# Optimization experiments

Hardware: AMD Instinct MI355X
Metric: run time of the kernel (lower is better)

Reference implementation:

```python
import jax, jax.numpy as jnp
import numpy as np

B, T, C = 4, 2048, 2048
H, N = 32, 64          # n_head, head_size; H*N == C (n_dim_att == n_dim)
DMIX, DDEC = 32, 64    # hardcoded LoRA dims in module


def setup_inputs() -> dict:
    key = jax.random.key(0)
    ks = jax.random.split(key, 24)
    u = lambda k, s, lo, hi: jax.random.uniform(k, s, jnp.float32, lo, hi)
    g = lambda k, s: jax.random.normal(k, s, jnp.float32) * 0.02
    return {
        'x': jax.random.normal(ks[0], (B, T, C), jnp.float32),
        'shift_state_in': jax.random.normal(ks[1], (B, C), jnp.float32),
        'wkv_state_in': jnp.zeros((B, H, N, N), jnp.float32),
        'time_maa_x': u(ks[2], (C,), 0.0, 1.0),
        'time_maa_r': u(ks[3], (C,), 0.0, 1.0),
        'time_maa_k': u(ks[4], (C,), 0.0, 1.0),
        'time_maa_v': u(ks[5], (C,), 0.0, 1.0),
        'time_maa_w': u(ks[6], (C,), 0.0, 1.0),
        'time_maa_v2': u(ks[7], (C,), 0.0, 1.0),
        'time_maa_w1': u(ks[8], (C, DMIX * 5), -0.01, 0.01),
        'time_maa_w2': u(ks[9], (5, DMIX, C), -0.01, 0.01),
        'time_decay': u(ks[10], (C,), -6.0, -1.0),
        'time_decay_w1': u(ks[11], (C, DDEC), -0.01, 0.01),
        'time_decay_w2': u(ks[12], (DDEC, C), -0.01, 0.01),
        'time_value2_w1': u(ks[13], (C, DDEC), -0.01, 0.01),
        'time_value2_w2': u(ks[14], (DDEC, C), -0.01, 0.01),
        'W_r': g(ks[15], (C, C)),
        'W_k': g(ks[16], (C, C)),
        'W_v': g(ks[17], (C, C)),
        'W_o': g(ks[18], (C, C)),
        'ln_w': jnp.ones((C,), jnp.float32),
        'ln_b': jnp.zeros((C,), jnp.float32),
    }


def _to_heads(a):
    # [B,T,C] -> [T,B,H,N] for time-major scan
    return a.reshape(B, T, H, N).transpose(1, 0, 2, 3)


def reference(x, shift_state_in, wkv_state_in,
              time_maa_x, time_maa_r, time_maa_k, time_maa_v, time_maa_w, time_maa_v2,
              time_maa_w1, time_maa_w2,
              time_decay, time_decay_w1, time_decay_w2,
              time_value2_w1, time_value2_w2,
              W_r, W_k, W_v, W_o, ln_w, ln_b):
    # token shift
    dxprev = jnp.concatenate([shift_state_in[:, None, :], x[:, :-1]], axis=1) - x
    xxx = x + dxprev * time_maa_x
    hmix = jnp.tanh(xxx @ time_maa_w1).reshape(B, T, 5, DMIX)
    mix = jnp.einsum('btfd,fdc->fbtc', hmix, time_maa_w2)  # [5,B,T,C]
    mr, mk, mv, mw, mv2 = mix
    xr = x + dxprev * (time_maa_r + mr)
    xk = x + dxprev * (time_maa_k + mk)
    xv = x + dxprev * (time_maa_v + mv)
    xw = x + dxprev * (time_maa_w + mw)
    xv2 = x + dxprev * (time_maa_v2 + mv2)

    r = xr @ W_r
    k = xk @ W_k
    v = xv @ W_v
    v2 = xv2 @ W_v + jnp.tanh(xv2 @ time_value2_w1) @ time_value2_w2
    w = time_decay + jnp.tanh(xw @ time_decay_w1) @ time_decay_w2
    decay = jnp.exp(-jnp.exp(w))         # per-channel, data-dependent
    k = k * (1.0 - decay)

    rh, kh, vh, dh = _to_heads(r), _to_heads(k), _to_heads(v), _to_heads(decay)

    def step(state, inputs):
        # state: [B,H,N,N] (k-dim x v-dim); u (time_faaaa) is zero in this variant
        r_t, k_t, v_t, d_t = inputs  # each [B,H,N]
        y = jnp.einsum('bhi,bhij->bhj', r_t, state)
        state = state * d_t[..., None] + k_t[..., None] * v_t[..., None, :]
        return state, y

    wkv_state_out, ys = jax.lax.scan(step, wkv_state_in, (rh, kh, vh, dh))
    y = ys.transpose(1, 0, 2, 3).reshape(B, T, C)
    y = y + v2
    # LayerNorm over n_dim_att
    mu = jnp.mean(y, axis=-1, keepdims=True)
    var = jnp.var(y, axis=-1, keepdims=True)
    y = (y - mu) / jnp.sqrt(var + 1e-5) * ln_w + ln_b
    y = y @ W_o
    return y, x[:, -1], wkv_state_out
```

## Files before the change

### kernel.cpp

```cpp
#include <hip/hip_runtime.h>
#include <hip/hip_bf16.h>
#include <cstdio>


typedef __attribute__((ext_vector_type(8))) short bf16x8;
typedef __attribute__((ext_vector_type(4))) float floatx4;

#define T_DIM 2048
#define C_DIM 2048
#define B_DIM 4
#define M_ROWS (B_DIM * T_DIM)

typedef const unsigned int __attribute__((address_space(1)))* gas1_t;
typedef unsigned int __attribute__((address_space(3)))* las3_t;
__device__ __forceinline__ void gl_lds16(const void* g, void* l) {
    __builtin_amdgcn_global_load_lds((gas1_t)g, (las3_t)l, 16, 0, 0);
}

__global__ __launch_bounds__(256) void k_transpose(
    const float* __restrict__ in, void* __restrict__ out,
    int R, int Cin, int to_bf16)
{
    __shared__ float tile[32][33];
    const int tx = threadIdx.x & 31, ty = threadIdx.x >> 5;
    const int cbase = blockIdx.x * 32, rbase = blockIdx.y * 32;
#pragma unroll
    for (int i = 0; i < 4; i++) {
        int r = rbase + ty + i * 8;
        int c = cbase + tx;
        tile[ty + i * 8][tx] = (c < Cin) ? in[(size_t)r * Cin + c] : 0.0f;
    }
    __syncthreads();
    if (to_bf16) {
        __hip_bfloat16* ob = (__hip_bfloat16*)out;
#pragma unroll
        for (int i = 0; i < 4; i++) {
            int c = cbase + ty + i * 8;
            ob[(size_t)c * R + rbase + tx] = __float2bfloat16(tile[tx][ty + i * 8]);
        }
    } else {
        float* of = (float*)out;
#pragma unroll
        for (int i = 0; i < 4; i++) {
            int c = cbase + ty + i * 8;
            of[(size_t)c * R + rbase + tx] = tile[tx][ty + i * 8];
        }
    }
}

__global__ __launch_bounds__(256) void k_xx(
    const float* __restrict__ x, const float* __restrict__ shift,
    const float* __restrict__ tmx,
    __hip_bfloat16* __restrict__ XX, float* __restrict__ xlast)
{
    const int row = blockIdx.x;
    const int b = row >> 11, t = row & 2047;
    const int c0 = threadIdx.x * 8;
    const float* xrow = x + (size_t)row * C_DIM;
    const float* prow = (t == 0) ? (shift + (size_t)b * C_DIM) : (xrow - C_DIM);
    float4 xa = ((const float4*)(xrow + c0))[0];
    float4 xb = ((const float4*)(xrow + c0))[1];
    float4 pa = ((const float4*)(prow + c0))[0];
    float4 pb = ((const float4*)(prow + c0))[1];
    float xv8[8] = {xa.x, xa.y, xa.z, xa.w, xb.x, xb.y, xb.z, xb.w};
    float pv8[8] = {pa.x, pa.y, pa.z, pa.w, pb.x, pb.y, pb.z, pb.w};
    union { bf16x8 v8; __hip_bfloat16 e[8]; } u;
#pragma unroll
    for (int j = 0; j < 8; j++)
        u.e[j] = __float2bfloat16(fmaf(pv8[j] - xv8[j], tmx[c0 + j], xv8[j]));
    *(bf16x8*)(XX + (size_t)row * C_DIM + c0) = u.v8;
    if (t == T_DIM - 1) {
        ((float4*)(xlast + (size_t)b * C_DIM + c0))[0] = xa;
        ((float4*)(xlast + (size_t)b * C_DIM + c0))[1] = xb;
    }
}

__global__ __launch_bounds__(256) void k_gemm_h(
    const __hip_bfloat16* __restrict__ A,
    const __hip_bfloat16* __restrict__ Bt,
    __hip_bfloat16* __restrict__ Hout)
{
    __shared__ __hip_bfloat16 As[64 * 32];
    __shared__ __hip_bfloat16 Bs[256 * 32];
    const int tid = threadIdx.x;
    const int m0 = blockIdx.x * 64;
    const int wave = tid >> 6, lane = tid & 63;
    const int fcol = lane & 15, quad = lane >> 4;
    floatx4 acc[16];
#pragma unroll
    for (int i = 0; i < 16; i++) acc[i] = (floatx4){0.f, 0.f, 0.f, 0.f};

    const int rA = tid >> 2, kcA = (tid & 3) * 8;
    const __hip_bfloat16* gA = A + (size_t)(m0 + rA) * 2048 + kcA;
    __hip_bfloat16* lA = As + tid * 8;
    const __hip_bfloat16* gB[4];
    __hip_bfloat16* lB[4];
#pragma unroll
    for (int s = 0; s < 4; s++) {
        int q = tid + 256 * s;
        gB[s] = Bt + (size_t)(q >> 2) * 2048 + (q & 3) * 8;
        lB[s] = Bs + q * 8;
    }
    for (int kk = 0; kk < 2048; kk += 32) {
        gl_lds16(gA + kk, lA);
#pragma unroll
        for (int s = 0; s < 4; s++) gl_lds16(gB[s] + kk, lB[s]);
        __syncthreads();
        bf16x8 aF = *(const bf16x8*)(As + (wave * 16 + fcol) * 32 + quad * 8);
#pragma unroll
        for (int ni = 0; ni < 16; ni++) {
            bf16x8 bF = *(const bf16x8*)(Bs + (ni * 16 + fcol) * 32 + quad * 8);
            acc[ni] = __builtin_amdgcn_mfma_f32_16x16x32_bf16(aF, bF, acc[ni], 0, 0, 0);
        }
        __syncthreads();
    }
#pragma unroll
    for (int ni = 0; ni < 16; ni++) {
        int col = ni * 16 + fcol;
#pragma unroll
        for (int g = 0; g < 4; g++) {
            int row = m0 + wave * 16 + quad * 4 + g;
            Hout[(size_t)row * 256 + col] = __float2bfloat16(tanhf(acc[ni][g]));
        }
    }
}

__global__ __launch_bounds__(256) void k_gemm_n64(
    const __hip_bfloat16* __restrict__ A,
    const __hip_bfloat16* __restrict__ Bt,
    __hip_bfloat16* __restrict__ G)
{
    __shared__ __hip_bfloat16 As[64 * 32];
    __shared__ __hip_bfloat16 Bs[64 * 32];
    const int tid = threadIdx.x;
    const int m0 = blockIdx.x * 64;
    const int wave = tid >> 6, lane = tid & 63;
    const int fcol = lane & 15, quad = lane >> 4;
    floatx4 acc[4];
#pragma unroll
    for (int i = 0; i < 4; i++) acc[i] = (floatx4){0.f, 0.f, 0.f, 0.f};

    const int r = tid >> 2, kc = (tid & 3) * 8;
    const __hip_bfloat16* gA = A + (size_t)(m0 + r) * 2048 + kc;
    const __hip_bfloat16* gB = Bt + (size_t)r * 2048 + kc;
    __hip_bfloat16* lA = As + tid * 8;
    __hip_bfloat16* lB = Bs + tid * 8;
    for (int kk = 0; kk < 2048; kk += 32) {
        gl_lds16(gA + kk, lA);
        gl_lds16(gB + kk, lB);
        __syncthreads();
        bf16x8 aF = *(const bf16x8*)(As + (wave * 16 + fcol) * 32 + quad * 8);
#pragma unroll
        for (int ni = 0; ni < 4; ni++) {
            bf16x8 bF = *(const bf16x8*)(Bs + (ni * 16 + fcol) * 32 + quad * 8);
            acc[ni] = __builtin_amdgcn_mfma_f32_16x16x32_bf16(aF, bF, acc[ni], 0, 0, 0);
        }
        __syncthreads();
    }
#pragma unroll
    for (int ni = 0; ni < 4; ni++) {
        int col = ni * 16 + fcol;
#pragma unroll
        for (int g = 0; g < 4; g++) {
            int row = m0 + wave * 16 + quad * 4 + g;
            G[(size_t)row * 64 + col] = __float2bfloat16(tanhf(acc[ni][g]));
        }
    }
}

__global__ __launch_bounds__(256) void k_mixfused(
    const float* __restrict__ x, const float* __restrict__ shift,
    const __hip_bfloat16* __restrict__ Hb,
    const __hip_bfloat16* __restrict__ w2T,
    const float* __restrict__ tmr, const float* __restrict__ tmk,
    const float* __restrict__ tmv, const float* __restrict__ tmw,
    const float* __restrict__ tmv2,
    __hip_bfloat16* __restrict__ xr, __hip_bfloat16* __restrict__ xk,
    __hip_bfloat16* __restrict__ xv, __hip_bfloat16* __restrict__ xw,
    __hip_bfloat16* __restrict__ xv2)
{
    __shared__ float          xp[33 * 256];
    __shared__ __hip_bfloat16 Hs[32 * 256];
    __shared__ __hip_bfloat16 mixS[32 * 256];

    const int tid = threadIdx.x;
    const int bid = blockIdx.x;
    const int n0 = (bid & 7) * 256;
    const int m0 = (bid >> 3) * 32;
    const int wave = tid >> 6, lane = tid & 63;
    const int fcol = lane & 15, quad = lane >> 4;
    const int wm = (wave >> 1) * 16, wn = (wave & 1) * 128;

#pragma unroll
    for (int i = 0; i < 8; i++) {
        int row = i * 4 + wave;
        gl_lds16(x + (size_t)(m0 + row) * C_DIM + n0 + lane * 4,
                 xp + (row + 1) * 256 + lane * 4);
    }
    if (wave == 0) {
        const float* src = (m0 & 2047)
            ? (x + (size_t)(m0 - 1) * C_DIM + n0)
            : (shift + (size_t)(m0 >> 11) * C_DIM + n0);
        gl_lds16(src + lane * 4, xp + lane * 4);
    }
#pragma unroll
    for (int i = 0; i < 4; i++) {
        int q = tid + 256 * i;
        gl_lds16(Hb + (size_t)(m0 + (q >> 5)) * 256 + (q & 31) * 8,
                 Hs + (q >> 5) * 256 + (q & 31) * 8);
    }
    asm volatile("s_waitcnt vmcnt(0) lgkmcnt(0)" ::: "memory");
    __builtin_amdgcn_s_barrier();
    __builtin_amdgcn_sched_barrier(0);

    const float* maas[5] = {tmr, tmk, tmv, tmw, tmv2};
    __hip_bfloat16* outs[5] = {xr, xk, xv, xw, xv2};
    const int cc = tid & 31, c0 = cc * 8, rb = tid >> 5;

#pragma unroll
    for (int f = 0; f < 5; f++) {
        {
            bf16x8 aF = *(const bf16x8*)(Hs + (wm + fcol) * 256 + f * 32 + quad * 8);
            floatx4 acc[8];
#pragma unroll
            for (int nf = 0; nf < 8; nf++) {
                bf16x8 bF = *(const bf16x8*)(
                    w2T + (size_t)(n0 + wn + nf * 16 + fcol) * 160 + f * 32 + quad * 8);
                acc[nf] = __builtin_amdgcn_mfma_f32_16x16x32_bf16(
                    aF, bF, (floatx4){0.f, 0.f, 0.f, 0.f}, 0, 0, 0);
            }
#pragma unroll
            for (int nf = 0; nf < 8; nf++)
#pragma unroll
                for (int g = 0; g < 4; g++)
                    mixS[(wm + quad * 4 + g) * 256 + wn + nf * 16 + fcol] =
                        __float2bfloat16(acc[nf][g]);
        }
        asm volatile("s_waitcnt lgkmcnt(0)" ::: "memory");
        __builtin_amdgcn_s_barrier();
        __builtin_amdgcn_sched_barrier(0);

        {
            float4 ma = ((const float4*)(maas[f] + n0 + c0))[0];
            float4 mb = ((const float4*)(maas[f] + n0 + c0))[1];
            float m8[8] = {ma.x, ma.y, ma.z, ma.w, mb.x, mb.y, mb.z, mb.w};
#pragma unroll
            for (int i = 0; i < 4; i++) {
                int row = rb + 8 * i;
                float4 xa = ((const float4*)(xp + (row + 1) * 256 + c0))[0];
                float4 xb = ((const float4*)(xp + (row + 1) * 256 + c0))[1];
                float4 pa = ((const float4*)(xp + row * 256 + c0))[0];
                float4 pb = ((const float4*)(xp + row * 256 + c0))[1];
                float xv8[8] = {xa.x, xa.y, xa.z, xa.w, xb.x, xb.y, xb.z, xb.w};
                float pv8[8] = {pa.x, pa.y, pa.z, pa.w, pb.x, pb.y, pb.z, pb.w};
                union { bf16x8 v8; __hip_bfloat16 e[8]; } mu;
                mu.v8 = *(const bf16x8*)(mixS + row * 256 + c0);
                union { bf16x8 v8; __hip_bfloat16 e[8]; } u;
#pragma unroll
                for (int j = 0; j < 8; j++) {
                    float dx = pv8[j] - xv8[j];
                    float mixv = __bfloat162float(mu.e[j]);
                    u.e[j] = __float2bfloat16(fmaf(dx, m8[j] + mixv, xv8[j]));
                }
                *(bf16x8*)(outs[f] + (size_t)(m0 + row) * C_DIM + n0 + c0) = u.v8;
            }
        }
        if (f < 4) {
            asm volatile("s_waitcnt lgkmcnt(0)" ::: "memory");
            __builtin_amdgcn_s_barrier();
            __builtin_amdgcn_sched_barrier(0);
        }
    }
}

__global__ __launch_bounds__(512, 2) void k_gemm256(
    const __hip_bfloat16* __restrict__ A,
    const __hip_bfloat16* __restrict__ Bt,
    int mode,
    float* __restrict__ outF, __hip_bfloat16* __restrict__ outB)
{
    constexpr int K = 2048;
    constexpr int NT = K / 32;
    __shared__ __hip_bfloat16 LA[4][256 * 32];
    __shared__ __hip_bfloat16 LB[4][256 * 32];
    const int tid = threadIdx.x;
    const int bid = blockIdx.x;
    const int n0 = (bid & 7) * 256;
    const int m0 = (bid >> 3) * 256;
    const int wave = tid >> 6, lane = tid & 63;
    const int wm = (wave >> 2) * 128, wn = (wave & 3) * 64;
    const int fcol = lane & 15, quad = lane >> 4;

    floatx4 acc[8][4];
#pragma unroll
    for (int mi = 0; mi < 8; mi++)
#pragma unroll
        for (int ni = 0; ni < 4; ni++)
            acc[mi][ni] = (floatx4){0.f, 0.f, 0.f, 0.f};

    const int ch0 = wave * 2, ch1 = wave * 2 + 1;
    const int rr = lane >> 2, kc = (lane & 3) * 8;
    const __hip_bfloat16* pA0 = A  + (size_t)(m0 + ch0 * 16 + rr) * K + kc;
    const __hip_bfloat16* pA1 = A  + (size_t)(m0 + ch1 * 16 + rr) * K + kc;
    const __hip_bfloat16* pB0 = Bt + (size_t)(n0 + ch0 * 16 + rr) * K + kc;
    const __hip_bfloat16* pB1 = Bt + (size_t)(n0 + ch1 * 16 + rr) * K + kc;
    const int lo0 = ch0 * 512 + lane * 8;
    const int lo1 = ch1 * 512 + lane * 8;

    int ns = 0;
    for (; ns < 3; ++ns) {
        gl_lds16(pA0 + ns * 32, &LA[ns][lo0]);
        gl_lds16(pA1 + ns * 32, &LA[ns][lo1]);
        gl_lds16(pB0 + ns * 32, &LB[ns][lo0]);
        gl_lds16(pB1 + ns * 32, &LB[ns][lo1]);
    }
    for (int t = 0; t < NT; ++t) {
        if (t < NT - 2)       asm volatile("s_waitcnt vmcnt(8)" ::: "memory");
        else if (t == NT - 2) asm volatile("s_waitcnt vmcnt(4)" ::: "memory");
        else                  asm volatile("s_waitcnt vmcnt(0)" ::: "memory");
        asm volatile("s_barrier" ::: "memory");
        if (ns < NT) {
            const int sl = ns & 3;
            gl_lds16(pA0 + ns * 32, &LA[sl][lo0]);
            gl_lds16(pA1 + ns * 32, &LA[sl][lo1]);
            gl_lds16(pB0 + ns * 32, &LB[sl][lo0]);
            gl_lds16(pB1 + ns * 32, &LB[sl][lo1]);
            ++ns;
        }
        const int st = t & 3;
        const __hip_bfloat16* ab = &LA[st][(wm + fcol) * 32 + quad * 8];
        const __hip_bfloat16* bb = &LB[st][(wn + fcol) * 32 + quad * 8];
        bf16x8 bF[4];
#pragma unroll
        for (int ni = 0; ni < 4; ni++)
            bF[ni] = *(const bf16x8*)(bb + ni * 512);
#pragma unroll
        for (int mi = 0; mi < 8; mi++) {
            bf16x8 aF = *(const bf16x8*)(ab + mi * 512);
#pragma unroll
            for (int ni = 0; ni < 4; ni++)
                acc[mi][ni] = __builtin_amdgcn_mfma_f32_16x16x32_bf16(
                    aF, bF[ni], acc[mi][ni], 0, 0, 0);
        }
    }
#pragma unroll
    for (int mi = 0; mi < 8; mi++) {
#pragma unroll
        for (int ni = 0; ni < 4; ni++) {
            int rbase = m0 + wm + mi * 16 + quad * 4;
            int ccol = n0 + wn + ni * 16 + fcol;
#pragma unroll
            for (int g = 0; g < 4; g++) {
                size_t idx = (size_t)(rbase + g) * 2048 + ccol;
                float val = acc[mi][ni][g];
                if (mode == 0) outF[idx] = val;
                else           outB[idx] = __float2bfloat16(val);
            }
        }
    }
}

__global__ __launch_bounds__(256) void k_gemm64(
    const __hip_bfloat16* __restrict__ A0, const __hip_bfloat16* __restrict__ B0,
    const __hip_bfloat16* __restrict__ A1, const __hip_bfloat16* __restrict__ B1,
    float* __restrict__ decayOut, const float* __restrict__ tdec,
    __hip_bfloat16* __restrict__ v2Out)
{
    constexpr int K = 64;
    __shared__ __hip_bfloat16 As[128 * 32];
    __shared__ __hip_bfloat16 Bs[128 * 32];
    const int tid = threadIdx.x;
    const int op = blockIdx.x >> 10;
    const int id = blockIdx.x & 1023;
    const int xcd = id & 7, jj = id >> 3;
    const int m0 = (((xcd << 3) | (jj & 7))) * 128;
    const int n0 = (jj >> 3) * 128;
    const __hip_bfloat16* A = op ? A1 : A0;
    const __hip_bfloat16* Bt = op ? B1 : B0;
    const int wave = tid >> 6, lane = tid & 63;
    const int wm = (wave >> 1) * 64, wn = (wave & 1) * 64;
    const int fcol = lane & 15, quad = lane >> 4;

    floatx4 acc[4][4];
#pragma unroll
    for (int mi = 0; mi < 4; mi++)
#pragma unroll
        for (int ni = 0; ni < 4; ni++)
            acc[mi][ni] = (floatx4){0.f, 0.f, 0.f, 0.f};

    const int q0 = tid, q1 = tid + 256;
    const int r0 = q0 >> 2, kc0 = (q0 & 3) * 8;
    const int r1 = q1 >> 2, kc1 = (q1 & 3) * 8;
    const __hip_bfloat16* gA0 = A + (size_t)(m0 + r0) * K + kc0;
    const __hip_bfloat16* gA1 = A + (size_t)(m0 + r1) * K + kc1;
    const __hip_bfloat16* gB0 = Bt + (size_t)(n0 + r0) * K + kc0;
    const __hip_bfloat16* gB1 = Bt + (size_t)(n0 + r1) * K + kc1;
    __hip_bfloat16* lA0 = As + q0 * 8; __hip_bfloat16* lA1 = As + q1 * 8;
    __hip_bfloat16* lB0 = Bs + q0 * 8; __hip_bfloat16* lB1 = Bs + q1 * 8;

    for (int kk = 0; kk < K; kk += 32) {
        gl_lds16(gA0 + kk, lA0);
        gl_lds16(gA1 + kk, lA1);
        gl_lds16(gB0 + kk, lB0);
        gl_lds16(gB1 + kk, lB1);
        __syncthreads();
        bf16x8 aF[4], bF[4];
#pragma unroll
        for (int mi = 0; mi < 4; mi++)
            aF[mi] = *(const bf16x8*)(As + (wm + mi * 16 + fcol) * 32 + quad * 8);
#pragma unroll
        for (int ni = 0; ni < 4; ni++)
            bF[ni] = *(const bf16x8*)(Bs + (wn + ni * 16 + fcol) * 32 + quad * 8);
#pragma unroll
        for (int mi = 0; mi < 4; mi++)
#pragma unroll
            for (int ni = 0; ni < 4; ni++)
                acc[mi][ni] = __builtin_amdgcn_mfma_f32_16x16x32_bf16(
                    aF[mi], bF[ni], acc[mi][ni], 0, 0, 0);
        __syncthreads();
    }
#pragma unroll
    for (int mi = 0; mi < 4; mi++) {
#pragma unroll
        for (int ni = 0; ni < 4; ni++) {
            int rbase = m0 + wm + mi * 16 + quad * 4;
            int ccol = n0 + wn + ni * 16 + fcol;
#pragma unroll
            for (int g = 0; g < 4; g++) {
                size_t idx = (size_t)(rbase + g) * 2048 + ccol;
                float val = acc[mi][ni][g];
                if (op == 0) {
                    decayOut[idx] = expf(-expf(val + tdec[ccol]));
                } else {
                    v2Out[idx] = __float2bfloat16(__bfloat162float(v2Out[idx]) + val);
                }
            }
        }
    }
}

__global__ __launch_bounds__(256) void k_scan_chunked(
    const __hip_bfloat16* __restrict__ r, const __hip_bfloat16* __restrict__ k,
    const __hip_bfloat16* __restrict__ v, const float* __restrict__ dec,
    const float* __restrict__ state_in,
    __hip_bfloat16* __restrict__ y, float* __restrict__ state_out)
{
    __shared__ __hip_bfloat16 Rs[2][64 * 64];
    __shared__ __hip_bfloat16 Ks[2][64 * 64];
    __shared__ __hip_bfloat16 Vs[2][64 * 64];
    __shared__ float          Dsb[2][64 * 64];
    __shared__ __hip_bfloat16 Ys[2][64 * 64];
    __shared__ __hip_bfloat16 Am[64 * 72];
    __shared__ __hip_bfloat16 Bm[64 * 72];
    __shared__ __hip_bfloat16 VT[64 * 72];
    __shared__ __hip_bfloat16 CT[64 * 72];
    __shared__ __hip_bfloat16 ST[64 * 72];
    __shared__ __hip_bfloat16 Pm[64 * 72];
    __shared__ float part[4][64];
    __shared__ float efin[64];

    const int tid = threadIdx.x;
    const int bh = blockIdx.x, b = bh >> 5, h = bh & 31;
    const int wave = tid >> 6, lane = tid & 63;
    const int fcol = lane & 15, quad = lane >> 4;
    const int ci = tid & 63, seg = tid >> 6;

    floatx4 sfr[4];
    {
        const float* sp = state_in + (size_t)bh * 4096;
#pragma unroll
        for (int n = 0; n < 4; n++)
#pragma unroll
            for (int g = 0; g < 4; g++)
                sfr[n][g] = sp[(size_t)(16 * wave + quad * 4 + g) * 64 + 16 * n + fcol];
    }

    const size_t cbase0 = (size_t)b * T_DIM * C_DIM + (size_t)h * 64;

    auto stage = [&](int cc, int buf) {
        const size_t cb = cbase0 + (size_t)cc * 64 * C_DIM;
        const int q0 = tid, q1 = tid + 256;
        const size_t o0 = (size_t)(q0 >> 3) * C_DIM + (q0 & 7) * 8;
        const size_t o1 = (size_t)(q1 >> 3) * C_DIM + (q1 & 7) * 8;
        gl_lds16(r + cb + o0, &Rs[buf][q0 * 8]);
        gl_lds16(r + cb + o1, &Rs[buf][q1 * 8]);
        gl_lds16(k + cb + o0, &Ks[buf][q0 * 8]);
        gl_lds16(k + cb + o1, &Ks[buf][q1 * 8]);
        gl_lds16(v + cb + o0, &Vs[buf][q0 * 8]);
        gl_lds16(v + cb + o1, &Vs[buf][q1 * 8]);
        gl_lds16(y + cb + o0, &Ys[buf][q0 * 8]);
        gl_lds16(y + cb + o1, &Ys[buf][q1 * 8]);
#pragma unroll
        for (int s = 0; s < 4; s++) {
            int q = tid + 256 * s;
            gl_lds16(dec + cb + (size_t)(q >> 4) * C_DIM + (q & 15) * 4,
                     &Dsb[buf][q * 4]);
        }
    };

    stage(0, 0);

    for (int c = 0; c < 32; c++) {
        const int cur = c & 1, nxt = cur ^ 1;
        const size_t cb = cbase0 + (size_t)c * 64 * C_DIM;

        if (c == 0) asm volatile("s_waitcnt vmcnt(0)" ::: "memory");
        else        asm volatile("s_waitcnt vmcnt(16)" ::: "memory");
        asm volatile("s_waitcnt lgkmcnt(0)" ::: "memory");
        __builtin_amdgcn_s_barrier();
        __builtin_amdgcn_sched_barrier(0);

        if (c + 1 < 32) stage(c + 1, nxt);

        {
#pragma unroll
            for (int n = 0; n < 4; n++)
#pragma unroll
                for (int g = 0; g < 4; g++)
                    ST[(size_t)(16 * n + fcol) * 72 + 16 * wave + quad * 4 + g] =
                        __float2bfloat16(sfr[n][g]);
            float p = 1.0f;
#pragma unroll
            for (int u = 0; u < 16; u++) p *= Dsb[cur][(seg * 16 + u) * 64 + ci];
            part[seg][ci] = p;
        }
        asm volatile("s_waitcnt lgkmcnt(0)" ::: "memory");
        __builtin_amdgcn_s_barrier();
        __builtin_amdgcn_sched_barrier(0);

        {
            float p0 = part[0][ci], p1 = part[1][ci], p2 = part[2][ci], p3 = part[3][ci];
            float pre = 1.0f;
            if (seg > 0) pre *= p0;
            if (seg > 1) pre *= p1;
            if (seg > 2) pre *= p2;
            float tot = p0 * p1 * p2 * p3;
            if (seg == 0) efin[ci] = tot;
            float e = pre;
#pragma unroll
            for (int u = 0; u < 16; u++) {
                int t = seg * 16 + u;
                float d = Dsb[cur][t * 64 + ci];
                float rv = __bfloat162float(Rs[cur][t * 64 + ci]);
                float kv = __bfloat162float(Ks[cur][t * 64 + ci]) * (1.0f - d);
                Am[t * 72 + ci] = __float2bfloat16(rv * e);
                e *= d;
                float bb = kv * __builtin_amdgcn_rcpf(e);
                Bm[t * 72 + ci] = __float2bfloat16(bb);
                CT[ci * 72 + t] = __float2bfloat16(bb * tot);
            }
#pragma unroll
            for (int u = 0; u < 16; u++) {
                int t = seg * 16 + ((u + (ci & 15)) & 15);
                VT[ci * 72 + t] = Vs[cur][t * 64 + ci];
            }
        }
        asm volatile("s_waitcnt lgkmcnt(0)" ::: "memory");
        __builtin_amdgcn_s_barrier();
        __builtin_amdgcn_sched_barrier(0);

        {
            bf16x8 af[2];
#pragma unroll
            for (int kk = 0; kk < 2; kk++)
                af[kk] = *(const bf16x8*)(Am + (16 * wave + fcol) * 72 + kk * 32 + quad * 8);
            floatx4 pfr[4], yfr[4];
#pragma unroll
            for (int n = 0; n < 4; n++) {
                pfr[n] = (floatx4){0.f, 0.f, 0.f, 0.f};
                yfr[n] = (floatx4){0.f, 0.f, 0.f, 0.f};
#pragma unroll
                for (int kk = 0; kk < 2; kk++) {
                    bf16x8 bF = *(const bf16x8*)(Bm + (16 * n + fcol) * 72 + kk * 32 + quad * 8);
                    bf16x8 sF = *(const bf16x8*)(ST + (16 * n + fcol) * 72 + kk * 32 + quad * 8);
                    pfr[n] = __builtin_amdgcn_mfma_f32_16x16x32_bf16(af[kk], bF, pfr[n], 0, 0, 0);
                    yfr[n] = __builtin_amdgcn_mfma_f32_16x16x32_bf16(af[kk], sF, yfr[n], 0, 0, 0);
                }
            }
#pragma unroll
            for (int n = 0; n < 4; n++)
#pragma unroll
                for (int g = 0; g < 4; g++) {
                    int t = 16 * wave + quad * 4 + g;
                    int s = 16 * n + fcol;
                    Pm[t * 72 + s] = (s < t) ? __float2bfloat16(pfr[n][g])
                                             : __float2bfloat16(0.0f);
                }
            float eg[4];
#pragma unroll
            for (int g = 0; g < 4; g++) eg[g] = efin[16 * wave + quad * 4 + g];
#pragma unroll
            for (int n = 0; n < 4; n++)
#pragma unroll
                for (int g = 0; g < 4; g++) sfr[n][g] *= eg[g];
            bf16x8 pf[2], cf[2];
#pragma unroll
            for (int kk = 0; kk < 2; kk++) {
                pf[kk] = *(const bf16x8*)(Pm + (16 * wave + fcol) * 72 + kk * 32 + quad * 8);
                cf[kk] = *(const bf16x8*)(CT + (16 * wave + fcol) * 72 + kk * 32 + quad * 8);
            }
#pragma unroll
            for (int n = 0; n < 4; n++) {
#pragma unroll
                for (int kk = 0; kk < 2; kk++) {
                    bf16x8 vF = *(const bf16x8*)(VT + (16 * n + fcol) * 72 + kk * 32 + quad * 8);
                    yfr[n] = __builtin_amdgcn_mfma_f32_16x16x32_bf16(pf[kk], vF, yfr[n], 0, 0, 0);
                    sfr[n] = __builtin_amdgcn_mfma_f32_16x16x32_bf16(cf[kk], vF, sfr[n], 0, 0, 0);
                }
            }
#pragma unroll
            for (int n = 0; n < 4; n++)
#pragma unroll
                for (int g = 0; g < 4; g++) {
                    int t = 16 * wave + quad * 4 + g;
                    int s = 16 * n + fcol;
                    size_t addr = cb + (size_t)t * C_DIM + s;
                    float yv = __bfloat162float(Ys[cur][t * 64 + s]) + yfr[n][g];
                    y[addr] = __float2bfloat16(yv);
                }
        }
    }
    {
        float* so = state_out + (size_t)bh * 4096;
#pragma unroll
        for (int n = 0; n < 4; n++)
#pragma unroll
            for (int g = 0; g < 4; g++)
                so[(size_t)(16 * wave + quad * 4 + g) * 64 + 16 * n + fcol] = sfr[n][g];
    }
}

__global__ __launch_bounds__(256) void k_addln(
    __hip_bfloat16* __restrict__ y,
    const float* __restrict__ lnw, const float* __restrict__ lnb)
{
    __shared__ float ls[4], ls2[4];
    const int row = blockIdx.x;
    const size_t base = (size_t)row * C_DIM;
    const int tid = threadIdx.x;
    const int c0 = tid * 8;
    union { bf16x8 v8; __hip_bfloat16 e[8]; } uin;
    uin.v8 = *(const bf16x8*)(y + base + c0);
    float vbuf[8];
#pragma unroll
    for (int j = 0; j < 8; j++) vbuf[j] = __bfloat162float(uin.e[j]);
    float s = 0.f, s2 = 0.f;
#pragma unroll
    for (int j = 0; j < 8; j++) { s += vbuf[j]; s2 += vbuf[j] * vbuf[j]; }
#pragma unroll
    for (int off = 32; off > 0; off >>= 1) {
        s += __shfl_down(s, off, 64);
        s2 += __shfl_down(s2, off, 64);
    }
    const int w = tid >> 6;
    if ((tid & 63) == 0) { ls[w] = s; ls2[w] = s2; }
    __syncthreads();
    float S = ls[0] + ls[1] + ls[2] + ls[3];
    float S2 = ls2[0] + ls2[1] + ls2[2] + ls2[3];
    float mu = S * (1.0f / C_DIM);
    float var = S2 * (1.0f / C_DIM) - mu * mu;
    float rs = rsqrtf(var + 1e-5f);
    union { bf16x8 v8; __hip_bfloat16 e[8]; } u;
#pragma unroll
    for (int j = 0; j < 8; j++) {
        int ccc = c0 + j;
        u.e[j] = __float2bfloat16((vbuf[j] - mu) * rs * lnw[ccc] + lnb[ccc]);
    }
    *(bf16x8*)(y + base + c0) = u.v8;
}

extern "C" void kernel_launch(void* const* d_in, const int* in_sizes, int n_in,
                              void* d_out, int out_size, void* d_ws, size_t ws_size,
                              hipStream_t stream)
{
    const float* x     = (const float*)d_in[0];
    const float* shift = (const float*)d_in[1];
    const float* wkvin = (const float*)d_in[2];
    const float* tmx   = (const float*)d_in[3];
    const float* tmr   = (const float*)d_in[4];
    const float* tmk   = (const float*)d_in[5];
    const float* tmv   = (const float*)d_in[6];
    const float* tmw   = (const float*)d_in[7];
    const float* tmv2  = (const float*)d_in[8];
    const float* w1    = (const float*)d_in[9];
    const float* w2    = (const float*)d_in[10];
    const float* tdec  = (const float*)d_in[11];
    const float* dw1   = (const float*)d_in[12];
    const float* dw2   = (const float*)d_in[13];
    const float* vw1   = (const float*)d_in[14];
    const float* vw2   = (const float*)d_in[15];
    const float* Wr    = (const float*)d_in[16];
    const float* Wk    = (const float*)d_in[17];
    const float* Wv    = (const float*)d_in[18];
    const float* Wo    = (const float*)d_in[19];
    const float* lnw   = (const float*)d_in[20];
    const float* lnb   = (const float*)d_in[21];

    const size_t SZ_XBF = (size_t)M_ROWS * C_DIM * 2;
    const size_t SZ_WBF = (size_t)C_DIM * C_DIM * 2;
    char* ws = (char*)d_ws;
    size_t off = 0;
    __hip_bfloat16* S0 = (__hip_bfloat16*)(ws + off); off += SZ_XBF;
    __hip_bfloat16* S1 = (__hip_bfloat16*)(ws + off); off += SZ_XBF;
    __hip_bfloat16* S2 = (__hip_bfloat16*)(ws + off); off += SZ_XBF;
    __hip_bfloat16* S3 = (__hip_bfloat16*)(ws + off); off += SZ_XBF;
    __hip_bfloat16* S4 = (__hip_bfloat16*)(ws + off); off += SZ_XBF;
    char* D = ws + off; off += (size_t)M_ROWS * C_DIM * 4;
    __hip_bfloat16* XX    = (__hip_bfloat16*)D;
    __hip_bfloat16* Hb    = (__hip_bfloat16*)(D + SZ_XBF);
    float*          decay = (float*)D;
    __hip_bfloat16* WrT = (__hip_bfloat16*)(ws + off); off += SZ_WBF;
    __hip_bfloat16* WkT = (__hip_bfloat16*)(ws + off); off += SZ_WBF;
    __hip_bfloat16* WvT = (__hip_bfloat16*)(ws + off); off += SZ_WBF;
    __hip_bfloat16* WoT = (__hip_bfloat16*)(ws + off); off += SZ_WBF;
    __hip_bfloat16* w1tb  = (__hip_bfloat16*)(ws + off); off += (size_t)256 * 2048 * 2;
    __hip_bfloat16* dw1t  = (__hip_bfloat16*)(ws + off); off += (size_t)64 * 2048 * 2;
    __hip_bfloat16* vw1t  = (__hip_bfloat16*)(ws + off); off += (size_t)64 * 2048 * 2;
    __hip_bfloat16* dw2t  = (__hip_bfloat16*)(ws + off); off += (size_t)2048 * 64 * 2;
    __hip_bfloat16* vw2t  = (__hip_bfloat16*)(ws + off); off += (size_t)2048 * 64 * 2;
    __hip_bfloat16* Gd    = (__hip_bfloat16*)(ws + off); off += (size_t)M_ROWS * 64 * 2;
    __hip_bfloat16* Gv    = (__hip_bfloat16*)(ws + off); off += (size_t)M_ROWS * 64 * 2;
    __hip_bfloat16* w2T   = (__hip_bfloat16*)(ws + off); off += (size_t)2048 * 160 * 2;
    if (ws_size < off) {
        fprintf(stderr, "kernel_launch: ws too small (%zu < %zu)\n", ws_size, off);
        return;
    }

    float* out_y     = (float*)d_out;
    float* out_xlast = out_y + (size_t)M_ROWS * C_DIM;
    float* out_state = out_xlast + (size_t)B_DIM * C_DIM;

    k_transpose<<<dim3(8, 64),  256, 0, stream>>>(w1,  w1tb, 2048, 160, 1);
    k_transpose<<<dim3(2, 64),  256, 0, stream>>>(dw1, dw1t, 2048, 64, 1);
    k_transpose<<<dim3(2, 64),  256, 0, stream>>>(vw1, vw1t, 2048, 64, 1);
    k_transpose<<<dim3(64, 2),  256, 0, stream>>>(dw2, dw2t, 64, 2048, 1);
    k_transpose<<<dim3(64, 2),  256, 0, stream>>>(vw2, vw2t, 64, 2048, 1);
    k_transpose<<<dim3(64, 5),  256, 0, stream>>>(w2,  w2T,  160, 2048, 1);
    k_transpose<<<dim3(64, 64), 256, 0, stream>>>(Wr, WrT, 2048, 2048, 1);
    k_transpose<<<dim3(64, 64), 256, 0, stream>>>(Wk, WkT, 2048, 2048, 1);
    k_transpose<<<dim3(64, 64), 256, 0, stream>>>(Wv, WvT, 2048, 2048, 1);
    k_transpose<<<dim3(64, 64), 256, 0, stream>>>(Wo, WoT, 2048, 2048, 1);

    k_xx<<<M_ROWS, 256, 0, stream>>>(x, shift, tmx, XX, out_xlast);
    k_gemm_h<<<128, 256, 0, stream>>>(XX, w1tb, Hb);
    k_mixfused<<<2048, 256, 0, stream>>>(x, shift, Hb, w2T,
                                         tmr, tmk, tmv, tmw, tmv2,
                                         S0, S1, S2, S3, S4);
    k_gemm_n64<<<128, 256, 0, stream>>>(S3, dw1t, Gd);
    k_gemm_n64<<<128, 256, 0, stream>>>(S4, vw1t, Gv);
    k_gemm256<<<256, 512, 0, stream>>>(S1, WkT, 1, nullptr, S3);
    k_gemm256<<<256, 512, 0, stream>>>(S0, WrT, 1, nullptr, S1);
    k_gemm256<<<256, 512, 0, stream>>>(S2, WvT, 1, nullptr, S0);
    k_gemm256<<<256, 512, 0, stream>>>(S4, WvT, 1, nullptr, S2);
    k_gemm64<<<2048, 256, 0, stream>>>(Gd, dw2t, Gv, vw2t, decay, tdec, S2);
    k_scan_chunked<<<128, 256, 0, stream>>>(S1, S3, S0, decay, wkvin, S2, out_state);
    k_addln<<<M_ROWS, 256, 0, stream>>>(S2, lnw, lnb);
    k_gemm256<<<256, 512, 0, stream>>>(S2, WoT, 0, out_y, nullptr);

    (void)in_sizes; (void)n_in; (void)out_size;
}
```

Baseline: 1.137 ms.

## Split chunked WKV scan across 8 waves per block instead of 4

Raises the chunked scan block from 256 to 512 threads. Each wave now owns a 16-row by 32-column slice of the state and output, and the per-chunk decay product and prep loops are split into 8 segments of 8 timesteps. The intra-chunk P matrix (A·Bᵀ) is computed redundantly by both column-half waves, and the staging loads and vmcnt wait are adjusted to match. Only 128 blocks run, so the goal is more latency hiding and parallelism per CU on the serial chunk loop, at the cost of duplicated MFMA work and more barrier participants.

Result: no change. 1.117 ms (-1.8%).

```diff
diff --git a/kernel.cpp b/kernel.cpp
--- a/kernel.cpp
+++ b/kernel.cpp
@@ -439,7 +439,7 @@
     }
 }
 
-__global__ __launch_bounds__(256) void k_scan_chunked(
+__global__ __launch_bounds__(512) void k_scan_chunked(
     const __hip_bfloat16* __restrict__ r, const __hip_bfloat16* __restrict__ k,
     const __hip_bfloat16* __restrict__ v, const float* __restrict__ dec,
     const float* __restrict__ state_in,
@@ -456,43 +456,39 @@
     __shared__ __hip_bfloat16 CT[64 * 72];
     __shared__ __hip_bfloat16 ST[64 * 72];
     __shared__ __hip_bfloat16 Pm[64 * 72];
-    __shared__ float part[4][64];
+    __shared__ float part[8][64];
     __shared__ float efin[64];
 
     const int tid = threadIdx.x;
     const int bh = blockIdx.x, b = bh >> 5, h = bh & 31;
     const int wave = tid >> 6, lane = tid & 63;
     const int fcol = lane & 15, quad = lane >> 4;
-    const int ci = tid & 63, seg = tid >> 6;
-
-    floatx4 sfr[4];
+    const int wr = wave & 3, wc = wave >> 2;
+    const int ci = lane, seg = wave;
+
+    floatx4 sfr[2];
     {
         const float* sp = state_in + (size_t)bh * 4096;
 #pragma unroll
-        for (int n = 0; n < 4; n++)
+        for (int n = 0; n < 2; n++)
 #pragma unroll
             for (int g = 0; g < 4; g++)
-                sfr[n][g] = sp[(size_t)(16 * wave + quad * 4 + g) * 64 + 16 * n + fcol];
+                sfr[n][g] = sp[(size_t)(16 * wr + quad * 4 + g) * 64
+                               + 32 * wc + 16 * n + fcol];
     }
 
     const size_t cbase0 = (size_t)b * T_DIM * C_DIM + (size_t)h * 64;
 
     auto stage = [&](int cc, int buf) {
         const size_t cb = cbase0 + (size_t)cc * 64 * C_DIM;
-        const int q0 = tid, q1 = tid + 256;
-        const size_t o0 = (size_t)(q0 >> 3) * C_DIM + (q0 & 7) * 8;
-        const size_t o1 = (size_t)(q1 >> 3) * C_DIM + (q1 & 7) * 8;
-        gl_lds16(r + cb + o0, &Rs[buf][q0 * 8]);
-        gl_lds16(r + cb + o1, &Rs[buf][q1 * 8]);
-        gl_lds16(k + cb + o0, &Ks[buf][q0 * 8]);
-        gl_lds16(k + cb + o1, &Ks[buf][q1 * 8]);
-        gl_lds16(v + cb + o0, &Vs[buf][q0 * 8]);
-        gl_lds16(v + cb + o1, &Vs[buf][q1 * 8]);
-        gl_lds16(y + cb + o0, &Ys[buf][q0 * 8]);
-        gl_lds16(y + cb + o1, &Ys[buf][q1 * 8]);
-#pragma unroll
-        for (int s = 0; s < 4; s++) {
-            int q = tid + 256 * s;
+        const size_t o = (size_t)(tid >> 3) * C_DIM + (tid & 7) * 8;
+        gl_lds16(r + cb + o, &Rs[buf][tid * 8]);
+        gl_lds16(k + cb + o, &Ks[buf][tid * 8]);
+        gl_lds16(v + cb + o, &Vs[buf][tid * 8]);
+        gl_lds16(y + cb + o, &Ys[buf][tid * 8]);
+#pragma unroll
+        for (int s = 0; s < 2; s++) {
+            int q = tid + 512 * s;
             gl_lds16(dec + cb + (size_t)(q >> 4) * C_DIM + (q & 15) * 4,
                      &Dsb[buf][q * 4]);
         }
@@ -505,7 +501,7 @@
         const size_t cb = cbase0 + (size_t)c * 64 * C_DIM;
 
         if (c == 0) asm volatile("s_waitcnt vmcnt(0)" ::: "memory");
-        else        asm volatile("s_waitcnt vmcnt(16)" ::: "memory");
+        else        asm volatile("s_waitcnt vmcnt(8)" ::: "memory");
         asm volatile("s_waitcnt lgkmcnt(0)" ::: "memory");
         __builtin_amdgcn_s_barrier();
         __builtin_amdgcn_sched_barrier(0);
@@ -514,14 +510,14 @@
 
         {
 #pragma unroll
-            for (int n = 0; n < 4; n++)
+            for (int n = 0; n < 2; n++)
 #pragma unroll
                 for (int g = 0; g < 4; g++)
-                    ST[(size_t)(16 * n + fcol) * 72 + 16 * wave + quad * 4 + g] =
-                        __float2bfloat16(sfr[n][g]);
+                    ST[(size_t)(32 * wc + 16 * n + fcol) * 72
+                       + 16 * wr + quad * 4 + g] = __float2bfloat16(sfr[n][g]);
             float p = 1.0f;
 #pragma unroll
-            for (int u = 0; u < 16; u++) p *= Dsb[cur][(seg * 16 + u) * 64 + ci];
+            for (int u = 0; u < 8; u++) p *= Dsb[cur][(seg * 8 + u) * 64 + ci];
             part[seg][ci] = p;
         }
         asm volatile("s_waitcnt lgkmcnt(0)" ::: "memory");
@@ -529,17 +525,19 @@
         __builtin_amdgcn_sched_barrier(0);
 
         {
-            float p0 = part[0][ci], p1 = part[1][ci], p2 = part[2][ci], p3 = part[3][ci];
+            float pp[8];
+#pragma unroll
+            for (int s = 0; s < 8; s++) pp[s] = part[s][ci];
             float pre = 1.0f;
-            if (seg > 0) pre *= p0;
-            if (seg > 1) pre *= p1;
-            if (seg > 2) pre *= p2;
-            float tot = p0 * p1 * p2 * p3;
+#pragma unroll
+            for (int s = 0; s < 7; s++) pre *= (s < seg) ? pp[s] : 1.0f;
+            float tot = pp[0] * pp[1] * pp[2] * pp[3]
+                      * pp[4] * pp[5] * pp[6] * pp[7];
             if (seg == 0) efin[ci] = tot;
             float e = pre;
 #pragma unroll
-            for (int u = 0; u < 16; u++) {
-                int t = seg * 16 + u;
+            for (int u = 0; u < 8; u++) {
+                int t = seg * 8 + u;
                 float d = Dsb[cur][t * 64 + ci];
                 float rv = __bfloat162float(Rs[cur][t * 64 + ci]);
                 float kv = __bfloat162float(Ks[cur][t * 64 + ci]) * (1.0f - d);
@@ -550,8 +548,8 @@
                 CT[ci * 72 + t] = __float2bfloat16(bb * tot);
             }
 #pragma unroll
-            for (int u = 0; u < 16; u++) {
-                int t = seg * 16 + ((u + (ci & 15)) & 15);
+            for (int u = 0; u < 8; u++) {
+                int t = seg * 8 + ((u + (ci & 7)) & 7);
                 VT[ci * 72 + t] = Vs[cur][t * 64 + ci];
             }
         }
@@ -563,59 +561,66 @@
             bf16x8 af[2];
 #pragma unroll
             for (int kk = 0; kk < 2; kk++)
-                af[kk] = *(const bf16x8*)(Am + (16 * wave + fcol) * 72 + kk * 32 + quad * 8);
-            floatx4 pfr[4], yfr[4];
-#pragma unroll
-            for (int n = 0; n < 4; n++) {
-                pfr[n] = (floatx4){0.f, 0.f, 0.f, 0.f};
+                af[kk] = *(const bf16x8*)(Am + (16 * wr + fcol) * 72 + kk * 32 + quad * 8);
+            floatx4 pfr[4];
+#pragma unroll
+            for (int n4 = 0; n4 < 4; n4++) {
+                pfr[n4] = (floatx4){0.f, 0.f, 0.f, 0.f};
+#pragma unroll
+                for (int kk = 0; kk < 2; kk++) {
+                    bf16x8 bF = *(const bf16x8*)(Bm + (16 * n4 + fcol) * 72 + kk * 32 + quad * 8);
+                    pfr[n4] = __builtin_amdgcn_mfma_f32_16x16x32_bf16(af[kk], bF, pfr[n4], 0, 0, 0);
+                }
+            }
+            floatx4 yfr[2];
+#pragma unroll
+            for (int n = 0; n < 2; n++) {
                 yfr[n] = (floatx4){0.f, 0.f, 0.f, 0.f};
 #pragma unroll
                 for (int kk = 0; kk < 2; kk++) {
-                    bf16x8 bF = *(const bf16x8*)(Bm + (16 * n + fcol) * 72 + kk * 32 + quad * 8);
-                    bf16x8 sF = *(const bf16x8*)(ST + (16 * n + fcol) * 72 + kk * 32 + quad * 8);
-                    pfr[n] = __builtin_amdgcn_mfma_f32_16x16x32_bf16(af[kk], bF, pfr[n], 0, 0, 0);
+                    bf16x8 sF = *(const bf16x8*)(ST + (32 * wc + 16 * n + fcol) * 72 + kk * 32 + quad * 8);
                     yfr[n] = __builtin_amdgcn_mfma_f32_16x16x32_bf16(af[kk], sF, yfr[n], 0, 0, 0);
                 }
             }
 #pragma unroll
-            for (int n = 0; n < 4; n++)
+            for (int n4 = 0; n4 < 4; n4++)
 #pragma unroll
                 for (int g = 0; g < 4; g++) {
-                    int t = 16 * wave + quad * 4 + g;
-                    int s = 16 * n + fcol;
-                    Pm[t * 72 + s] = (s < t) ? __float2bfloat16(pfr[n][g])
+                    int t = 16 * wr + quad * 4 + g;
+                    int s = 16 * n4 + fcol;
+                    Pm[t * 72 + s] = (s < t) ? __float2bfloat16(pfr[n4][g])
                                              : __float2bfloat16(0.0f);
                 }
             float eg[4];
 #pragma unroll
-            for (int g = 0; g < 4; g++) eg[g] = efin[16 * wave + quad * 4 + g];
-#pragma unroll
-            for (int n = 0; n < 4; n++)
+            for (int g = 0; g < 4; g++) eg[g] = efin[16 * wr + quad * 4 + g];
+#pragma unroll
+            for (int n = 0; n < 2; n++)
 #pragma unroll
                 for (int g = 0; g < 4; g++) sfr[n][g] *= eg[g];
             bf16x8 pf[2], cf[2];
 #pragma unroll
             for (int kk = 0; kk < 2; kk++) {
-                pf[kk] = *(const bf16x8*)(Pm + (16 * wave + fcol) * 72 + kk * 32 + quad * 8);
-                cf[kk] = *(const bf16x8*)(CT + (16 * wave + fcol) * 72 + kk * 32 + quad * 8);
-            }
-#pragma unroll
-            for (int n = 0; n < 4; n++) {
+                pf[kk] = *(const bf16x8*)(Pm + (16 * wr + fcol) * 72 + kk * 32 + quad * 8);
+                cf[kk] = *(const bf16x8*)(CT + (16 * wr + fcol) * 72 + kk * 32 + quad * 8);
+            }
+#pragma unroll
+            for (int n = 0; n < 2; n++) {
 #pragma unroll
                 for (int kk = 0; kk < 2; kk++) {
-                    bf16x8 vF = *(const bf16x8*)(VT + (16 * n + fcol) * 72 + kk * 32 + quad * 8);
+                    bf16x8 vF = *(const bf16x8*)(VT + (32 * wc + 16 * n + fcol) * 72 + kk * 32 + quad * 8);
                     yfr[n] = __builtin_amdgcn_mfma_f32_16x16x32_bf16(pf[kk], vF, yfr[n], 0, 0, 0);
                     sfr[n] = __builtin_amdgcn_mfma_f32_16x16x32_bf16(cf[kk], vF, sfr[n], 0, 0, 0);
                 }
             }
 #pragma unroll
-            for (int n = 0; n < 4; n++)
+            for (int n = 0; n < 2; n++)
 #pragma unroll
                 for (int g = 0; g < 4; g++) {
-                    int t = 16 * wave + quad * 4 + g;
-                    int s = 16 * n + fcol;
-                    size_t addr = cb + (size_t)t * C_DIM + s;
-                    float yv = __bfloat162float(Ys[cur][t * 64 + s]) + yfr[n][g];
+                    int t = 16 * wr + quad * 4 + g;
+                    int j = 32 * wc + 16 * n + fcol;
+                    size_t addr = cb + (size_t)t * C_DIM + j;
+                    float yv = __bfloat162float(Ys[cur][t * 64 + j]) + yfr[n][g];
                     y[addr] = __float2bfloat16(yv);
                 }
         }
@@ -623,10 +628,11 @@
     {
         float* so = state_out + (size_t)bh * 4096;
 #pragma unroll
-        for (int n = 0; n < 4; n++)
+        for (int n = 0; n < 2; n++)
 #pragma unroll
             for (int g = 0; g < 4; g++)
-                so[(size_t)(16 * wave + quad * 4 + g) * 64 + 16 * n + fcol] = sfr[n][g];
+                so[(size_t)(16 * wr + quad * 4 + g) * 64 + 32 * wc + 16 * n + fcol]
+                    = sfr[n][g];
     }
 }
 
@@ -753,7 +759,7 @@
     k_gemm256<<<256, 512, 0, stream>>>(S2, WvT, 1, nullptr, S0);
     k_gemm256<<<256, 512, 0, stream>>>(S4, WvT, 1, nullptr, S2);
     k_gemm64<<<2048, 256, 0, stream>>>(Gd, dw2t, Gv, vw2t, decay, tdec, S2);
-    k_scan_chunked<<<128, 256, 0, stream>>>(S1, S3, S0, decay, wkvin, S2, out_state);
+    k_scan_chunked<<<128, 512, 0, stream>>>(S1, S3, S0, decay, wkvin, S2, out_state);
     k_addln<<<M_ROWS, 256, 0, stream>>>(S2, lnw, lnb);
     k_gemm256<<<256, 512, 0, stream>>>(S2, WoT, 0, out_y, nullptr);
 
```
